# Kernel tuning notes

Hardware: AMD Instinct MI355X
Metric: run time of the kernel (lower is better)

The kernel has to match this reference:

```python
import jax, jax.numpy as jnp
import numpy as np

N_HEADS = 12


def setup_inputs() -> dict:
    key = jax.random.key(0)
    ks = jax.random.split(key, 5)
    B, T, D = 4, 2048, 768
    std = 1.0 / np.sqrt(D)
    return {
        "x": jax.random.normal(ks[0], (B, T, D), jnp.float32),
        "W_qkv": jax.random.normal(ks[1], (3 * D, D), jnp.float32) * std,
        "b_qkv": jax.random.normal(ks[2], (3 * D,), jnp.float32) * 0.02,
        "W_proj": jax.random.normal(ks[3], (D, D), jnp.float32) * std,
        "b_proj": jax.random.normal(ks[4], (D,), jnp.float32) * 0.02,
    }


def reference(x, W_qkv, b_qkv, W_proj, b_proj):
    # x: [B, T, D]; intended 3D path of the module (dropout = eval-mode identity)
    B, T, D = x.shape
    H = N_HEADS
    Dh = D // H
    scale = Dh ** -0.5
    qkv = x @ W_qkv.T + b_qkv                       # [B, T, 3D]
    qkv = qkv.reshape(B, T, 3, H, Dh)
    q = jnp.transpose(qkv[:, :, 0], (0, 2, 1, 3))    # [B, H, T, Dh]
    k = jnp.transpose(qkv[:, :, 1], (0, 2, 1, 3))
    v = jnp.transpose(qkv[:, :, 2], (0, 2, 1, 3))
    attn = jnp.einsum("bhqd,bhkd->bhqk", q, k) * scale  # [B, H, T, T]
    scores = jax.nn.softmax(attn, axis=-1)
    out = jnp.einsum("bhqk,bhkd->bhqd", scores, v)       # [B, H, T, Dh]
    out = jnp.transpose(out, (0, 2, 1, 3)).reshape(B, T, D)
    return out @ W_proj.T + b_proj
```

## Files before the change

### kernel.cpp

```cpp
#include <hip/hip_runtime.h>
#include <hip/hip_bf16.h>
#include <stdint.h>

typedef __bf16 bf16;
typedef __bf16 bf16x8 __attribute__((ext_vector_type(8)));
typedef __bf16 bf16x4 __attribute__((ext_vector_type(4)));
typedef short  s16x4  __attribute__((ext_vector_type(4)));
typedef short  s16x8  __attribute__((ext_vector_type(8)));
typedef float  f32x4  __attribute__((ext_vector_type(4)));

#define N_B 4
#define N_T 2048
#define N_D 768
#define N_H 12
#define N_DH 64
#define M_TOT (N_B * N_T)

__device__ __forceinline__ void async_copy16(const bf16* g, bf16* l) {
    __builtin_amdgcn_global_load_lds(
        (const __attribute__((address_space(1))) unsigned int*)g,
        (__attribute__((address_space(3))) unsigned int*)l,
        16, 0, 0);
}

__launch_bounds__(256)
__global__ void f2bf3(const float* __restrict__ a, bf16* __restrict__ oa, int na,
                      const float* __restrict__ b, bf16* __restrict__ ob, int nb,
                      const float* __restrict__ c, bf16* __restrict__ oc) {
    int i = (blockIdx.x * 256 + threadIdx.x) * 4;
    const float* src; bf16* dst;
    if (i < na)            { src = a; dst = oa; }
    else if (i < na + nb)  { src = b; dst = ob; i -= na; }
    else                   { src = c; dst = oc; i -= na + nb; }
    const float4 v = *(const float4*)(src + i);
    bf16x4 o;
    o[0] = (bf16)v.x; o[1] = (bf16)v.y; o[2] = (bf16)v.z; o[3] = (bf16)v.w;
    *(bf16x4*)(dst + i) = o;
}

#define GEMM_STAGE(P, K0)                                                      \
    _Pragma("unroll")                                                          \
    for (int jj = 0; jj < 4; jj++)                                             \
        async_copy16(Ab + (size_t)jj * 32 * KD + (K0), &lsA[P][(jj * 256 + t) * 8]); \
    _Pragma("unroll")                                                          \
    for (int jj = 0; jj < TN / 32; jj++)                                       \
        async_copy16(Bb + (size_t)jj * 32 * KD + (K0), &lsB[P][(jj * 256 + t) * 8]);

#define GEMM_CORE(A_PTR, B_PTR, KDIM, TN_)                                     \
    constexpr int KD = (KDIM);                                                 \
    constexpr int TN = (TN_);                                                  \
    constexpr int JJ = TN / 32;                                                \
    constexpr int NT = KD / 64;                                                \
    __shared__ bf16 lsA[2][128 * 64];                                          \
    __shared__ bf16 lsB[2][TN * 64];                                           \
    const int m0 = blockIdx.x * 128;                                           \
    const int n0 = blockIdx.y * TN;                                            \
    const int t  = threadIdx.x;                                                \
    const int w  = t >> 6, l = t & 63;                                         \
    const int wm = w & 1, wn = w >> 1;                                         \
    const int lr = l & 15, lq = l >> 4;                                        \
    f32x4 acc[4][JJ] = {};                                                     \
    const int cs = (t & 7) ^ ((t >> 3) & 7);                                   \
    const bf16* Ab = (A_PTR) + (size_t)(m0 + (t >> 3)) * KD + cs * 8;          \
    const bf16* Bb = (B_PTR) + (size_t)(n0 + (t >> 3)) * KD + cs * 8;          \
    GEMM_STAGE(0, 0)                                                           \
    for (int t0 = 0; t0 < NT; t0++) {                                          \
        const int p = t0 & 1;                                                  \
        __syncthreads();                                                       \
        if (t0 + 1 < NT) { GEMM_STAGE(p ^ 1, (t0 + 1) * 64) }                  \
        _Pragma("unroll")                                                      \
        for (int ks = 0; ks < 2; ks++) {                                       \
            bf16x8 af[4], bfr[JJ];                                             \
            _Pragma("unroll")                                                  \
            for (int i = 0; i < 4; i++)                                        \
                af[i] = *(const bf16x8*)(&lsA[p][(wm * 64 + i * 16 + lr) * 64  \
                                         + (((ks * 4 + lq) ^ (lr & 7)) * 8)]); \
            _Pragma("unroll")                                                  \
            for (int j = 0; j < JJ; j++)                                       \
                bfr[j] = *(const bf16x8*)(&lsB[p][(wn * (TN / 2) + j * 16 + lr) * 64 \
                                          + (((ks * 4 + lq) ^ (lr & 7)) * 8)]); \
            _Pragma("unroll")                                                  \
            for (int i = 0; i < 4; i++)                                        \
                _Pragma("unroll")                                              \
                for (int j = 0; j < JJ; j++)                                   \
                    acc[i][j] = __builtin_amdgcn_mfma_f32_16x16x32_bf16(       \
                        af[i], bfr[j], acc[i][j], 0, 0, 0);                    \
        }                                                                      \
    }

__launch_bounds__(256)
__global__ void gemm_qkv(const bf16* __restrict__ X, const bf16* __restrict__ W,
                         const float* __restrict__ bias,
                         bf16* __restrict__ Q, bf16* __restrict__ K,
                         bf16* __restrict__ Vt) {
    GEMM_CORE(X, W, 768, 128)
    for (int i = 0; i < 4; i++) {
        const int rowb = m0 + wm * 64 + i * 16 + lq * 4;
        const int b_ = rowb >> 11, tt = rowb & 2047;
        for (int j = 0; j < 4; j++) {
            const int col   = n0 + wn * 64 + j * 16 + lr;
            const int which = col / 768;
            const int rem   = col - which * 768;
            const int h     = rem >> 6, d = rem & 63;
            const float bv  = bias[col];
            if (which == 2) {
                const int tile = tt >> 6, kl = tt & 63;
                const int ki = kl >> 4, lqv = (kl >> 2) & 3;
                const int idx = 32 * (ki & 1) + 8 * lqv + 4 * (ki >> 1);
                bf16x4 v4;
                for (int r2 = 0; r2 < 4; r2++) v4[r2] = (bf16)(acc[i][j][r2] + bv);
                *(bf16x4*)(Vt + ((size_t)((b_ * N_H + h) * 64 + d)) * 2048
                           + tile * 64 + idx) = v4;
            } else {
                bf16* dst = (which == 0) ? Q : K;
                const float sc = (which == 0) ? 0.18033688f : 1.0f;
                for (int r2 = 0; r2 < 4; r2++)
                    dst[(size_t)(((b_ * N_H + h) << 11) + tt + r2) * 64 + d] =
                        (bf16)((acc[i][j][r2] + bv) * sc);
            }
        }
    }
}

__launch_bounds__(256)
__global__ void gemm_proj(const bf16* __restrict__ O, const bf16* __restrict__ W,
                          const float* __restrict__ bias, float* __restrict__ out) {
    GEMM_CORE(O, W, 768, 64)
    for (int i = 0; i < 4; i++) {
        const int rowb = m0 + wm * 64 + i * 16 + lq * 4;
        for (int j = 0; j < JJ; j++) {
            const int col  = n0 + wn * (TN / 2) + j * 16 + lr;
            const float bv = bias[col];
            for (int r = 0; r < 4; r++)
                out[(size_t)(rowb + r) * 768 + col] = acc[i][j][r] + bv;
        }
    }
}

__launch_bounds__(256, 3)
__global__ void attn(const bf16* __restrict__ Q, const bf16* __restrict__ K,
                     const bf16* __restrict__ Vt, bf16* __restrict__ O) {
    __shared__ bf16 lsK[3][64 * 64];
    __shared__ bf16 lsV[3][64 * 64];
    const int bid = blockIdx.x;
    const int xcd = bid & 7, slot = bid >> 3;
    const int bh  = xcd + 8 * (slot >> 4);
    const int qt  = slot & 15;
    const int t = threadIdx.x, w = t >> 6, l = t & 63;
    const int lr = l & 15, lq = l >> 4;
    const bf16* Qh  = Q  + (size_t)bh * N_T * 64;
    const bf16* Kh  = K  + (size_t)bh * N_T * 64;
    const bf16* Vth = Vt + (size_t)bh * 64 * N_T;
    const int q0 = qt * 128 + w * 32;

    bf16x8 qf[2][2];
    #pragma unroll
    for (int qg = 0; qg < 2; qg++)
        #pragma unroll
        for (int ks = 0; ks < 2; ks++)
            qf[qg][ks] = *(const bf16x8*)(Qh + (size_t)(q0 + qg * 16 + lr) * 64
                                          + ks * 32 + lq * 8);

    f32x4 oacc[2][4] = {};
    f32x4 lacc[2]    = {};
    const bf16x8 ones8 = {(bf16)1.f, (bf16)1.f, (bf16)1.f, (bf16)1.f,
                          (bf16)1.f, (bf16)1.f, (bf16)1.f, (bf16)1.f};

    #pragma unroll
    for (int tile = 0; tile < 2; tile++)
        #pragma unroll
        for (int j = 0; j < 2; j++) {
            const int u   = t + j * 256;
            const int row = u >> 3;
            const int scn = (u & 7) ^ (row & 7);
            async_copy16(Kh  + (size_t)(tile * 64 + row) * 64 + scn * 8,
                         lsK[tile] + u * 8);
            async_copy16(Vth + (size_t)row * 2048 + tile * 64 + scn * 8,
                         lsV[tile] + u * 8);
        }

    int cur = 0;
    for (int kt = 0; kt < 32; kt++) {
        if (kt < 31)
            asm volatile("s_waitcnt vmcnt(4) lgkmcnt(0)\n\ts_barrier" ::: "memory");
        else
            asm volatile("s_waitcnt vmcnt(0) lgkmcnt(0)\n\ts_barrier" ::: "memory");

        if (kt < 30) {
            int nb = cur + 2; if (nb >= 3) nb -= 3;
            #pragma unroll
            for (int j = 0; j < 2; j++) {
                const int u   = t + j * 256;
                const int row = u >> 3;
                const int scn = (u & 7) ^ (row & 7);
                async_copy16(Kh + (size_t)((kt + 2) * 64 + row) * 64 + scn * 8,
                             lsK[nb] + u * 8);
                async_copy16(Vth + (size_t)row * 2048 + (kt + 2) * 64 + scn * 8,
                             lsV[nb] + u * 8);
            }
        }

        bf16x8 kf[2][4];
        #pragma unroll
        for (int ks = 0; ks < 2; ks++)
            #pragma unroll
            for (int ki = 0; ki < 4; ki++) {
                const int row = ki * 16 + lr;
                kf[ks][ki] = *(const bf16x8*)(lsK[cur] + row * 64
                                              + ((ks * 4 + lq) ^ (lr & 7)) * 8);
            }

        bf16x8 pbf[2][2];
        #pragma unroll
        for (int qg = 0; qg < 2; qg++) {
            f32x4 sacc[4] = {};
            __builtin_amdgcn_s_setprio(1);
            #pragma unroll
            for (int ks = 0; ks < 2; ks++)
                #pragma unroll
                for (int ki = 0; ki < 4; ki++)
                    sacc[ki] = __builtin_amdgcn_mfma_f32_16x16x32_bf16(
                        kf[ks][ki], qf[qg][ks], sacc[ki], 0, 0, 0);
            __builtin_amdgcn_s_setprio(0);
            #pragma unroll
            for (int ks = 0; ks < 2; ks++) {
                bf16x8 pb;
                #pragma unroll
                for (int r = 0; r < 4; r++) {
                    pb[r]     = (bf16)exp2f(sacc[ks][r]);
                    pb[4 + r] = (bf16)exp2f(sacc[ks + 2][r]);
                }
                pbf[qg][ks] = pb;
            }
        }

        __builtin_amdgcn_s_setprio(1);
        #pragma unroll
        for (int ks = 0; ks < 2; ks++)
            #pragma unroll
            for (int dj = 0; dj < 4; dj++) {
                const int row  = dj * 16 + lr;
                const int unit = (4 * ks + lq) ^ (lr & 7);
                bf16x8 vf = *(const bf16x8*)(lsV[cur] + row * 64 + unit * 8);
                #pragma unroll
                for (int qg = 0; qg < 2; qg++)
                    oacc[qg][dj] = __builtin_amdgcn_mfma_f32_16x16x32_bf16(
                        vf, pbf[qg][ks], oacc[qg][dj], 0, 0, 0);
            }
        #pragma unroll
        for (int qg = 0; qg < 2; qg++)
            #pragma unroll
            for (int ks = 0; ks < 2; ks++)
                lacc[qg] = __builtin_amdgcn_mfma_f32_16x16x32_bf16(
                    ones8, pbf[qg][ks], lacc[qg], 0, 0, 0);
        __builtin_amdgcn_s_setprio(0);

        cur = cur + 1; if (cur == 3) cur = 0;
    }

    const int b = bh / N_H, h = bh - b * N_H;
    #pragma unroll
    for (int qg = 0; qg < 2; qg++) {
        const float inv_l = 1.0f / lacc[qg][0];
        const int tok = q0 + qg * 16 + lr;
        bf16* Ob = O + ((size_t)b * N_T + tok) * N_D + h * 64;
        #pragma unroll
        for (int dj = 0; dj < 4; dj++) {
            bf16x4 o4;
            #pragma unroll
            for (int r = 0; r < 4; r++) o4[r] = (bf16)(oacc[qg][dj][r] * inv_l);
            *(bf16x4*)(Ob + dj * 16 + lq * 4) = o4;
        }
    }
}

extern "C" void kernel_launch(void* const* d_in, const int* in_sizes, int n_in,
                              void* d_out, int out_size, void* d_ws, size_t ws_size,
                              hipStream_t stream) {
    const float* x      = (const float*)d_in[0];
    const float* W_qkv  = (const float*)d_in[1];
    const float* b_qkv  = (const float*)d_in[2];
    const float* W_proj = (const float*)d_in[3];
    const float* b_proj = (const float*)d_in[4];
    float* out = (float*)d_out;

    char* ws = (char*)d_ws;
    const size_t n_x  = (size_t)M_TOT * N_D;
    const size_t n_wq = (size_t)3 * N_D * N_D;
    const size_t n_wp = (size_t)N_D * N_D;
    const size_t sz_qkv = (size_t)N_B * N_H * N_T * N_DH * sizeof(bf16);

    bf16* xb  = (bf16*)(ws);                 ws += n_x * sizeof(bf16);
    bf16* Wqb = (bf16*)(ws);                 ws += n_wq * sizeof(bf16);
    bf16* Wpb = (bf16*)(ws);                 ws += n_wp * sizeof(bf16);
    bf16* Qb  = (bf16*)(ws);                 ws += sz_qkv;
    bf16* Kb  = (bf16*)(ws);                 ws += sz_qkv;
    bf16* Vtb = (bf16*)(ws);                 ws += sz_qkv;
    bf16* Ob  = (bf16*)(ws);

    dim3 blk(256);
    f2bf3<<<dim3((int)((n_x + n_wq + n_wp) / 1024)), blk, 0, stream>>>(
        x, xb, (int)n_x, W_qkv, Wqb, (int)n_wq, W_proj, Wpb);

    gemm_qkv<<<dim3(M_TOT / 128, 2304 / 128), blk, 0, stream>>>(xb, Wqb, b_qkv, Qb, Kb, Vtb);
    attn<<<dim3(768), dim3(256), 0, stream>>>(Qb, Kb, Vtb, Ob);
    gemm_proj<<<dim3(M_TOT / 128, 768 / 64), blk, 0, stream>>>(Ob, Wpb, b_proj, out);
}
```

Measured before the change: 222.0 us.

## Prefetch two K-tiles ahead in GEMM core with explicit vmcnt waits

Restructures the shared GEMM main loop so two stages are issued before the loop starts. Each iteration reads all LDS fragments into registers first, then refills the same buffer with the tile two steps ahead before running the MFMAs. Explicit s_waitcnt vmcnt/lgkmcnt plus s_barrier replace __syncthreads, so global loads can stay in flight across a full compute step. This costs more fragment registers and relies on hand-counted vmcnt values that must match the number of async copies per stage.

Measured after the change: 216.5 us. 1.03x faster.

```diff
diff --git a/kernel.cpp b/kernel.cpp
--- a/kernel.cpp
+++ b/kernel.cpp
@@ -15,6 +15,9 @@
 #define N_H 12
 #define N_DH 64
 #define M_TOT (N_B * N_T)
+
+#define GSTR2(x) #x
+#define GSTR(x) GSTR2(x)
 
 __device__ __forceinline__ void async_copy16(const bf16* g, bf16* l) {
     __builtin_amdgcn_global_load_lds(
@@ -46,7 +49,7 @@
     for (int jj = 0; jj < TN / 32; jj++)                                       \
         async_copy16(Bb + (size_t)jj * 32 * KD + (K0), &lsB[P][(jj * 256 + t) * 8]);
 
-#define GEMM_CORE(A_PTR, B_PTR, KDIM, TN_)                                     \
+#define GEMM_CORE(A_PTR, B_PTR, KDIM, TN_, VMC)                                \
     constexpr int KD = (KDIM);                                                 \
     constexpr int TN = (TN_);                                                  \
     constexpr int JJ = TN / 32;                                                \
@@ -64,27 +67,37 @@
     const bf16* Ab = (A_PTR) + (size_t)(m0 + (t >> 3)) * KD + cs * 8;          \
     const bf16* Bb = (B_PTR) + (size_t)(n0 + (t >> 3)) * KD + cs * 8;          \
     GEMM_STAGE(0, 0)                                                           \
+    GEMM_STAGE(1, 64)                                                          \
+    asm volatile("s_waitcnt vmcnt(" GSTR(VMC) ")\n\ts_barrier" ::: "memory");  \
     for (int t0 = 0; t0 < NT; t0++) {                                          \
         const int p = t0 & 1;                                                  \
-        __syncthreads();                                                       \
-        if (t0 + 1 < NT) { GEMM_STAGE(p ^ 1, (t0 + 1) * 64) }                  \
+        bf16x8 af[2][4], bfr[2][JJ];                                           \
         _Pragma("unroll")                                                      \
         for (int ks = 0; ks < 2; ks++) {                                       \
-            bf16x8 af[4], bfr[JJ];                                             \
             _Pragma("unroll")                                                  \
             for (int i = 0; i < 4; i++)                                        \
-                af[i] = *(const bf16x8*)(&lsA[p][(wm * 64 + i * 16 + lr) * 64  \
-                                         + (((ks * 4 + lq) ^ (lr & 7)) * 8)]); \
+                af[ks][i] = *(const bf16x8*)(&lsA[p][(wm * 64 + i * 16 + lr) * 64 \
+                                             + (((ks * 4 + lq) ^ (lr & 7)) * 8)]); \
             _Pragma("unroll")                                                  \
             for (int j = 0; j < JJ; j++)                                       \
-                bfr[j] = *(const bf16x8*)(&lsB[p][(wn * (TN / 2) + j * 16 + lr) * 64 \
-                                          + (((ks * 4 + lq) ^ (lr & 7)) * 8)]); \
+                bfr[ks][j] = *(const bf16x8*)(&lsB[p][(wn * (TN / 2) + j * 16 + lr) * 64 \
+                                              + (((ks * 4 + lq) ^ (lr & 7)) * 8)]); \
+        }                                                                      \
+        asm volatile("s_waitcnt lgkmcnt(0)\n\ts_barrier" ::: "memory");        \
+        if (t0 + 2 < NT) { GEMM_STAGE(p, (t0 + 2) * 64) }                      \
+        _Pragma("unroll")                                                      \
+        for (int ks = 0; ks < 2; ks++)                                         \
             _Pragma("unroll")                                                  \
             for (int i = 0; i < 4; i++)                                        \
                 _Pragma("unroll")                                              \
                 for (int j = 0; j < JJ; j++)                                   \
                     acc[i][j] = __builtin_amdgcn_mfma_f32_16x16x32_bf16(       \
-                        af[i], bfr[j], acc[i][j], 0, 0, 0);                    \
+                        af[ks][i], bfr[ks][j], acc[i][j], 0, 0, 0);            \
+        if (t0 + 1 < NT) {                                                     \
+            if (t0 + 2 < NT)                                                   \
+                asm volatile("s_waitcnt vmcnt(" GSTR(VMC) ")\n\ts_barrier" ::: "memory"); \
+            else                                                               \
+                asm volatile("s_waitcnt vmcnt(0)\n\ts_barrier" ::: "memory");  \
         }                                                                      \
     }
 
@@ -93,11 +106,11 @@
                          const float* __restrict__ bias,
                          bf16* __restrict__ Q, bf16* __restrict__ K,
                          bf16* __restrict__ Vt) {
-    GEMM_CORE(X, W, 768, 128)
+    GEMM_CORE(X, W, 768, 128, 8)
     for (int i = 0; i < 4; i++) {
         const int rowb = m0 + wm * 64 + i * 16 + lq * 4;
         const int b_ = rowb >> 11, tt = rowb & 2047;
-        for (int j = 0; j < 4; j++) {
+        for (int j = 0; j < JJ; j++) {
             const int col   = n0 + wn * 64 + j * 16 + lr;
             const int which = col / 768;
             const int rem   = col - which * 768;
@@ -125,7 +138,7 @@
 __launch_bounds__(256)
 __global__ void gemm_proj(const bf16* __restrict__ O, const bf16* __restrict__ W,
                           const float* __restrict__ bias, float* __restrict__ out) {
-    GEMM_CORE(O, W, 768, 64)
+    GEMM_CORE(O, W, 768, 64, 6)
     for (int i = 0; i < 4; i++) {
         const int rowb = m0 + wm * 64 + i * 16 + lq * 4;
         for (int j = 0; j < JJ; j++) {
```
